# Kernel optimization log

Measured on AMD Instinct MI355X. Metric: run time of the kernel, lower is better.

## Reference

```python
import jax, jax.numpy as jnp
import numpy as np

EPS = 1e-5

def _bn_train(h, gamma, beta):
    # BatchNorm1d in training mode: batch mean and biased variance over batch dim
    mu = jnp.mean(h, axis=0)
    var = jnp.mean((h - mu) ** 2, axis=0)
    return (h - mu) * jax.lax.rsqrt(var + EPS) * gamma + beta

def setup_inputs() -> dict:
    key = jax.random.key(0)
    ks = jax.random.split(key, 12)
    B, IN, H1, H2, NC = 16384, 4096, 256, 128, 12
    x = jax.random.normal(ks[0], (B, 1, 64, 64), dtype=jnp.float32)
    y = jax.random.randint(ks[1], (B,), 0, NC, dtype=jnp.int32)
    s1 = 1.0 / np.sqrt(IN)
    W1 = jax.random.uniform(ks[2], (H1, IN), jnp.float32, -s1, s1)
    b1 = jax.random.uniform(ks[3], (H1,), jnp.float32, -s1, s1)
    g1 = jax.random.normal(ks[4], (H1,), jnp.float32) * 0.1 + 1.0
    be1 = jax.random.normal(ks[5], (H1,), jnp.float32) * 0.1
    s2 = 1.0 / np.sqrt(H1)
    W2 = jax.random.uniform(ks[6], (H2, H1), jnp.float32, -s2, s2)
    b2 = jax.random.uniform(ks[7], (H2,), jnp.float32, -s2, s2)
    g2 = jax.random.normal(ks[8], (H2,), jnp.float32) * 0.1 + 1.0
    be2 = jax.random.normal(ks[9], (H2,), jnp.float32) * 0.1
    s4 = 1.0 / np.sqrt(H2)
    W4 = jax.random.uniform(ks[10], (NC, H2), jnp.float32, -s4, s4)
    b4 = jax.random.uniform(ks[11], (NC,), jnp.float32, -s4, s4)
    return {"x": x, "W1": W1, "b1": b1, "g1": g1, "be1": be1,
            "W2": W2, "b2": b2, "g2": g2, "be2": be2,
            "W4": W4, "b4": b4, "y": y}

def reference(x, W1, b1, g1, be1, W2, b2, g2, be2, W4, b4, y):
    B = x.shape[0]
    h = x.reshape(B, -1)  # [B, 4096]
    # layer 1: binarized linear + BN(train) + hardtanh (dropout p=0 is identity)
    h = h @ jnp.sign(W1).T + jnp.sign(b1)
    h = jnp.clip(_bn_train(h, g1, be1), -1.0, 1.0)
    # layer 2
    h = h @ jnp.sign(W2).T + jnp.sign(b2)
    h = jnp.clip(_bn_train(h, g2, be2), -1.0, 1.0)
    # final float linear
    return h @ W4.T + b4  # [B, 12]
```

## Files before the change

### kernel.cpp

```cpp
#include <hip/hip_runtime.h>
#include <cstddef>

typedef __attribute__((ext_vector_type(8))) short short8;
typedef __attribute__((ext_vector_type(4))) float f4;
typedef __attribute__((ext_vector_type(4))) unsigned int u4;

__device__ __forceinline__ unsigned int f2bf(float f){
  unsigned int u = __float_as_uint(f);
  u += 0x7fffu + ((u >> 16) & 1u);
  return u >> 16;
}
__device__ __forceinline__ float bflo(unsigned int w){ return __uint_as_float((w & 0xFFFFu) << 16); }
__device__ __forceinline__ float bfhi(unsigned int w){ return __uint_as_float(w & 0xFFFF0000u); }
__device__ __forceinline__ float fsign(float x){ return (x > 0.f) ? 1.f : ((x < 0.f) ? -1.f : 0.f); }
__device__ __forceinline__ float hclip(float x){ return fminf(1.f, fmaxf(-1.f, x)); }

#define SB0 __builtin_amdgcn_sched_barrier(0)

#define BARRIER() do { \
    SB0; \
    asm volatile("s_waitcnt lgkmcnt(0)" ::: "memory"); \
    __builtin_amdgcn_s_barrier(); \
    asm volatile("" ::: "memory"); \
    SB0; \
  } while(0)

#define VBAR(N) do { \
    SB0; \
    asm volatile("s_waitcnt vmcnt(" #N ") lgkmcnt(0)" ::: "memory"); \
    __builtin_amdgcn_s_barrier(); \
    asm volatile("" ::: "memory"); \
    SB0; \
  } while(0)

#define GL16(gp, lp) __builtin_amdgcn_global_load_lds( \
    (const __attribute__((address_space(1))) void*)(gp), \
    (__attribute__((address_space(3))) void*)(lp), 16, 0, 0)

__global__ void prep_sign_k(const float* __restrict__ W1, unsigned short* __restrict__ w1s,
                            const float* __restrict__ W2, unsigned short* __restrict__ w2s){
  int i = (blockIdx.x * blockDim.x + threadIdx.x) * 8;
  const float* w; unsigned short* o; int off;
  if (i < 1048576){ w = W1; o = w1s; off = i; }
  else            { w = W2; o = w2s; off = i - 1048576; if (off >= 32768) return; }
  f4 a = *(const f4*)(w + off);
  f4 b = *(const f4*)(w + off + 4);
  unsigned short s[8];
  #pragma unroll
  for (int j = 0; j < 4; j++) s[j]   = (a[j] > 0.f) ? 0x3F80u : ((a[j] < 0.f) ? 0xBF80u : 0u);
  #pragma unroll
  for (int j = 0; j < 4; j++) s[4+j] = (b[j] > 0.f) ? 0x3F80u : ((b[j] < 0.f) ? 0xBF80u : 0u);
  u4 v;
  v.x = (unsigned)s[0] | ((unsigned)s[1] << 16);
  v.y = (unsigned)s[2] | ((unsigned)s[3] << 16);
  v.z = (unsigned)s[4] | ((unsigned)s[5] << 16);
  v.w = (unsigned)s[6] | ((unsigned)s[7] << 16);
  *(u4*)(o + off) = v;
}

__global__ __launch_bounds__(512, 1) void gemm1_k(
    const float* __restrict__ x, const unsigned short* __restrict__ w1s,
    const float* __restrict__ b1, unsigned short* __restrict__ h1,
    float* __restrict__ part1s, float* __restrict__ part1q)
{
  __shared__ __align__(16) char lds[147456];
  const int tid  = threadIdx.x;
  const int lane = tid & 63;
  const int wid  = tid >> 6;
  const int wm   = wid >> 2;
  const int wn   = wid & 3;
  const int cl   = lane & 15;
  const int g    = lane >> 4;
  const int row0 = blockIdx.x * 64;

  const float* xA = x + (size_t)(row0 + (tid >> 3)) * 4096 + (tid & 7) * 8;
  const int aw = (tid >> 3) * 128 + (((tid & 7) * 16) ^ (((tid >> 3) & 7) << 4));

  int afo[2][2], bfo[4][2];
  #pragma unroll
  for (int fm = 0; fm < 2; fm++){
    int m = wm * 32 + fm * 16 + cl;
    #pragma unroll
    for (int ks = 0; ks < 2; ks++)
      afo[fm][ks] = m * 128 + ((ks * 64 + g * 16) ^ ((m & 7) << 4));
  }
  #pragma unroll
  for (int fn = 0; fn < 4; fn++){
    int n = wn * 64 + fn * 16 + cl;
    #pragma unroll
    for (int ks = 0; ks < 2; ks++)
      bfo[fn][ks] = n * 128 + ((ks * 64 + g * 16) ^ ((n & 7) << 4));
  }

  f4 acc[2][4];
  const f4 z = {0.f, 0.f, 0.f, 0.f};
  #pragma unroll
  for (int i = 0; i < 2; i++)
    #pragma unroll
    for (int j = 0; j < 4; j++) acc[i][j] = z;

  f4 rA0a, rA0b, rA1a, rA1b, rA2a, rA2b, rA3a, rA3b;

#define ISSUEA(S, K) do { \
    rA##S##a = *(const f4*)(xA + (size_t)(K) * 64); \
    rA##S##b = *(const f4*)(xA + (size_t)(K) * 64 + 4); \
  } while(0)

#define ISSUEB(BI, K) do { \
    char* _dst = lds + 16384 + (BI) * 32768; \
    _Pragma("unroll") \
    for (int _c = 0; _c < 4; _c++){ \
      int _o  = _c * 8192 + tid * 16; \
      int _n  = _o >> 7; \
      int _kb = (_o & 127) ^ ((_n & 7) << 4); \
      GL16((const char*)w1s + (size_t)_n * 8192 + (size_t)(K) * 128 + _kb, _dst + _o); \
    } } while(0)

#define PACKA(S, AB) do { \
    u4 _v; \
    _v.x = f2bf(rA##S##a[0]) | (f2bf(rA##S##a[1]) << 16); \
    _v.y = f2bf(rA##S##a[2]) | (f2bf(rA##S##a[3]) << 16); \
    _v.z = f2bf(rA##S##b[0]) | (f2bf(rA##S##b[1]) << 16); \
    _v.w = f2bf(rA##S##b[2]) | (f2bf(rA##S##b[3]) << 16); \
    *(u4*)(lds + (AB) * 8192 + aw) = _v; \
  } while(0)

#define COMPUTE(KI) do { \
    const char* _ab = lds + ((KI) & 1) * 8192; \
    const char* _bb = lds + 16384 + ((KI) & 3) * 32768; \
    short8 _af[2][2]; short8 _bf[4][2]; \
    _Pragma("unroll") \
    for (int _fm = 0; _fm < 2; _fm++) \
      _Pragma("unroll") \
      for (int _ks = 0; _ks < 2; _ks++) \
        _af[_fm][_ks] = *(const short8*)(_ab + afo[_fm][_ks]); \
    _Pragma("unroll") \
    for (int _fn = 0; _fn < 4; _fn++) \
      _Pragma("unroll") \
      for (int _ks = 0; _ks < 2; _ks++) \
        _bf[_fn][_ks] = *(const short8*)(_bb + bfo[_fn][_ks]); \
    __builtin_amdgcn_s_setprio(1); \
    _Pragma("unroll") \
    for (int _ks = 0; _ks < 2; _ks++) \
      _Pragma("unroll") \
      for (int _fm = 0; _fm < 2; _fm++) \
        _Pragma("unroll") \
        for (int _fn = 0; _fn < 4; _fn++) \
          acc[_fm][_fn] = __builtin_amdgcn_mfma_f32_16x16x32_bf16(_af[_fm][_ks], _bf[_fn][_ks], acc[_fm][_fn], 0, 0, 0); \
    __builtin_amdgcn_s_setprio(0); \
  } while(0)

#define STEP(K, AS, AP) do { \
    int _kb3 = (K) + 3; if (_kb3 > 63) _kb3 = 63; \
    int _ka4 = (K) + 4; if (_ka4 > 63) _ka4 = 63; \
    ISSUEB((K + 3) & 3, _kb3); \
    ISSUEA(AS, _ka4); \
    SB0; \
    COMPUTE(K); \
    SB0; \
    if ((K) < 63) PACKA(AP, ((K) + 1) & 1); \
    VBAR(14); \
  } while(0)

  ISSUEA(0, 0);
  ISSUEB(0, 0); ISSUEB(1, 1); ISSUEB(2, 2);
  ISSUEA(1, 1); ISSUEA(2, 2); ISSUEA(3, 3);
  SB0;
  PACKA(0, 0);
  VBAR(14);

  #pragma unroll 1
  for (int kk = 0; kk < 64; kk += 4){
    STEP(kk + 0, 0, 1);
    STEP(kk + 1, 1, 2);
    STEP(kk + 2, 2, 3);
    STEP(kk + 3, 3, 0);
  }
  asm volatile("s_waitcnt vmcnt(0)" ::: "memory");

#undef STEP
#undef COMPUTE
#undef PACKA
#undef ISSUEB
#undef ISSUEA

  #pragma unroll
  for (int fn = 0; fn < 4; fn++){
    int c = wn * 64 + fn * 16 + cl;
    float sb = fsign(b1[c]);
    float s = 0.f, q = 0.f;
    #pragma unroll
    for (int fm = 0; fm < 2; fm++){
      int rbase = row0 + wm * 32 + fm * 16 + g * 4;
      #pragma unroll
      for (int i = 0; i < 4; i++){
        float v = acc[fm][fn][i] + sb;
        h1[(size_t)(rbase + i) * 256 + c] = (unsigned short)f2bf(v);
        s += v; q += v * v;
      }
    }
    s += __shfl_xor(s, 16, 64); s += __shfl_xor(s, 32, 64);
    q += __shfl_xor(q, 16, 64); q += __shfl_xor(q, 32, 64);
    if (g == 0){
      part1s[(size_t)c * 512 + blockIdx.x * 2 + wm] = s;
      part1q[(size_t)c * 512 + blockIdx.x * 2 + wm] = q;
    }
  }
}

template<int COLS, int NBLK>
__global__ __launch_bounds__(64) void params_k(
    const float* __restrict__ ps, const float* __restrict__ pq,
    const float* __restrict__ g, const float* __restrict__ be,
    float* __restrict__ ab){
  int j = blockIdx.x * 64 + threadIdx.x;
  const f4* vs = (const f4*)(ps + (size_t)j * NBLK);
  const f4* vq = (const f4*)(pq + (size_t)j * NBLK);
  f4 s4 = {0,0,0,0}, q4 = {0,0,0,0};
  #pragma unroll 8
  for (int b = 0; b < NBLK/4; b++){ s4 += vs[b]; q4 += vq[b]; }
  float s = s4[0]+s4[1]+s4[2]+s4[3];
  float q = q4[0]+q4[1]+q4[2]+q4[3];
  float mu  = s * (1.f/16384.f);
  float var = q * (1.f/16384.f) - mu*mu;
  float a   = g[j] * rsqrtf(var + 1e-5f);
  ab[j] = a;
  ab[COLS + j] = be[j] - mu*a;
}

__global__ __launch_bounds__(512) void gemm2_k(
    const unsigned short* __restrict__ h1, const unsigned short* __restrict__ w2s,
    const float* __restrict__ b2, const float* __restrict__ ab1,
    unsigned short* __restrict__ h2, float* __restrict__ part2s, float* __restrict__ part2q)
{
  __shared__ __align__(16) char lds[32768];
  __shared__ __align__(16) float a1l[256];
  __shared__ __align__(16) float c1l[256];
  const int tid  = threadIdx.x;
  const int lane = tid & 63;
  const int wid  = tid >> 6;
  const int cl   = lane & 15;
  const int g    = lane >> 4;
  const int klo  = g * 8;
  const int row0 = blockIdx.x * 64;

  if (tid < 256) a1l[tid] = ab1[tid];
  else           c1l[tid - 256] = ab1[tid];

  const int am  = tid >> 3;
  const int ak0 = (tid & 7) * 8;
  const unsigned short* hA = h1 + (size_t)(row0 + am) * 256 + ak0;
  const int aw = ((am * 128) + (ak0 * 2)) ^ ((am & 7) << 4);
  const unsigned short* wbase = w2s + (size_t)(wid * 16 + cl) * 256 + klo;

  u4 q0 = *(const u4*)(hA);
  u4 q1 = *(const u4*)(hA + 64);
  u4 q2 = *(const u4*)(hA + 128);
  u4 q3 = *(const u4*)(hA + 192);
  short8 Bq0, Bq1, Br0, Br1;
  Bq0 = *(const short8*)(wbase);
  Bq1 = *(const short8*)(wbase + 32);

  BARRIER();

#define TRW(KB, RAW) do { \
    f4 _a0 = *(const f4*)(&a1l[(KB)*64 + ak0]); \
    f4 _a1 = *(const f4*)(&a1l[(KB)*64 + ak0 + 4]); \
    f4 _c0 = *(const f4*)(&c1l[(KB)*64 + ak0]); \
    f4 _c1 = *(const f4*)(&c1l[(KB)*64 + ak0 + 4]); \
    float _t0 = hclip(_a0[0]*bflo(RAW.x) + _c0[0]); \
    float _t1 = hclip(_a0[1]*bfhi(RAW.x) + _c0[1]); \
    float _t2 = hclip(_a0[2]*bflo(RAW.y) + _c0[2]); \
    float _t3 = hclip(_a0[3]*bfhi(RAW.y) + _c0[3]); \
    float _t4 = hclip(_a1[0]*bflo(RAW.z) + _c1[0]); \
    float _t5 = hclip(_a1[1]*bfhi(RAW.z) + _c1[1]); \
    float _t6 = hclip(_a1[2]*bflo(RAW.w) + _c1[2]); \
    float _t7 = hclip(_a1[3]*bfhi(RAW.w) + _c1[3]); \
    u4 _v; \
    _v.x = f2bf(_t0) | (f2bf(_t1) << 16); \
    _v.y = f2bf(_t2) | (f2bf(_t3) << 16); \
    _v.z = f2bf(_t4) | (f2bf(_t5) << 16); \
    _v.w = f2bf(_t6) | (f2bf(_t7) << 16); \
    *(u4*)(lds + (KB)*8192 + aw) = _v; \
  } while(0)

  TRW(0, q0); TRW(1, q1); TRW(2, q2); TRW(3, q3);
#undef TRW
  BARRIER();

  f4 acc[4];
  const f4 z = {0.f, 0.f, 0.f, 0.f};
  #pragma unroll
  for (int i = 0; i < 4; i++) acc[i] = z;

#define LOADB2(P, KB) do { \
    B##P##0 = *(const short8*)(wbase + (KB)*64); \
    B##P##1 = *(const short8*)(wbase + (KB)*64 + 32); \
  } while(0)

#define COMP2(BASE, P) do { \
    const char* _ab = (const char*)(BASE); \
    short8 _af[4][2]; \
    _Pragma("unroll") \
    for (int fm = 0; fm < 4; fm++){ \
      int _m = fm*16 + cl; \
      _af[fm][0] = *(const short8*)(_ab + ((_m*128 + klo*2) ^ ((_m & 7) << 4))); \
      _af[fm][1] = *(const short8*)(_ab + ((_m*128 + (32 + klo)*2) ^ ((_m & 7) << 4))); \
    } \
    _Pragma("unroll") \
    for (int fm = 0; fm < 4; fm++){ \
      acc[fm] = __builtin_amdgcn_mfma_f32_16x16x32_bf16(_af[fm][0], B##P##0, acc[fm], 0, 0, 0); \
      acc[fm] = __builtin_amdgcn_mfma_f32_16x16x32_bf16(_af[fm][1], B##P##1, acc[fm], 0, 0, 0); \
    } \
  } while(0)

  LOADB2(r, 1);
  COMP2(lds,         q);
  LOADB2(q, 2);
  COMP2(lds +  8192, r);
  LOADB2(r, 3);
  COMP2(lds + 16384, q);
  COMP2(lds + 24576, r);
#undef COMP2
#undef LOADB2

  {
    int c = wid*16 + cl;
    float sb = fsign(b2[c]);
    float s = 0.f, q = 0.f;
    #pragma unroll
    for (int fm = 0; fm < 4; fm++){
      int rbase = row0 + fm*16 + g*4;
      #pragma unroll
      for (int i = 0; i < 4; i++){
        float v = acc[fm][i] + sb;
        h2[(size_t)(rbase + i)*128 + c] = (unsigned short)f2bf(v);
        s += v; q += v*v;
      }
    }
    s += __shfl_xor(s, 16, 64); s += __shfl_xor(s, 32, 64);
    q += __shfl_xor(q, 16, 64); q += __shfl_xor(q, 32, 64);
    if (g == 0){
      part2s[c*256 + blockIdx.x] = s;
      part2q[c*256 + blockIdx.x] = q;
    }
  }
}

__global__ __launch_bounds__(128) void final_k(
    const unsigned short* __restrict__ h2,
    const float* __restrict__ part2s, const float* __restrict__ part2q,
    const float* __restrict__ g2, const float* __restrict__ be2,
    const float* __restrict__ W4, const float* __restrict__ b4,
    float* __restrict__ out)
{
  __shared__ __align__(16) float W4l[12*128];
  __shared__ __align__(16) float a2l[128];
  __shared__ __align__(16) float c2l[128];
  const int t = threadIdx.x;
  #pragma unroll
  for (int i = 0; i < 3; i++)
    *(f4*)&W4l[(i*128 + t)*4] = *(const f4*)(W4 + (i*128 + t)*4);
  {
    const f4* vs = (const f4*)(part2s + t*256);
    const f4* vq = (const f4*)(part2q + t*256);
    f4 s4 = {0,0,0,0}, q4 = {0,0,0,0};
    #pragma unroll 8
    for (int b = 0; b < 64; b++){ s4 += vs[b]; q4 += vq[b]; }
    float s = s4[0]+s4[1]+s4[2]+s4[3];
    float q = q4[0]+q4[1]+q4[2]+q4[3];
    float mu  = s * (1.f/16384.f);
    float var = q * (1.f/16384.f) - mu*mu;
    float a   = g2[t] * rsqrtf(var + 1e-5f);
    a2l[t] = a;
    c2l[t] = be2[t] - mu*a;
  }
  __syncthreads();

  const int r = blockIdx.x * 128 + t;
  const u4* hp = (const u4*)(h2 + (size_t)r * 128);
  u4 hv0 = hp[0], hv1 = hp[1], hv2 = hp[2],  hv3 = hp[3];
  u4 hv4 = hp[4], hv5 = hp[5], hv6 = hp[6],  hv7 = hp[7];
  u4 hv8 = hp[8], hv9 = hp[9], hv10 = hp[10], hv11 = hp[11];
  u4 hv12 = hp[12], hv13 = hp[13], hv14 = hp[14], hv15 = hp[15];

  float acc[12];
  #pragma unroll
  for (int o = 0; o < 12; o++) acc[o] = b4[o];

#define FPROC(HV, J) do { \
    f4 a0 = *(const f4*)&a2l[(J)*8];     f4 a1 = *(const f4*)&a2l[(J)*8 + 4]; \
    f4 c0 = *(const f4*)&c2l[(J)*8];     f4 c1 = *(const f4*)&c2l[(J)*8 + 4]; \
    float tt0 = hclip(a0[0]*bflo(HV.x) + c0[0]); \
    float tt1 = hclip(a0[1]*bfhi(HV.x) + c0[1]); \
    float tt2 = hclip(a0[2]*bflo(HV.y) + c0[2]); \
    float tt3 = hclip(a0[3]*bfhi(HV.y) + c0[3]); \
    float tt4 = hclip(a1[0]*bflo(HV.z) + c1[0]); \
    float tt5 = hclip(a1[1]*bfhi(HV.z) + c1[1]); \
    float tt6 = hclip(a1[2]*bflo(HV.w) + c1[2]); \
    float tt7 = hclip(a1[3]*bfhi(HV.w) + c1[3]); \
    _Pragma("unroll") \
    for (int o = 0; o < 12; o++){ \
      f4 w0 = *(const f4*)&W4l[o*128 + (J)*8]; \
      f4 w1 = *(const f4*)&W4l[o*128 + (J)*8 + 4]; \
      acc[o] += tt0*w0[0] + tt1*w0[1] + tt2*w0[2] + tt3*w0[3] \
              + tt4*w1[0] + tt5*w1[1] + tt6*w1[2] + tt7*w1[3]; \
    } \
  } while(0)

  FPROC(hv0, 0);  FPROC(hv1, 1);  FPROC(hv2, 2);   FPROC(hv3, 3);
  FPROC(hv4, 4);  FPROC(hv5, 5);  FPROC(hv6, 6);   FPROC(hv7, 7);
  FPROC(hv8, 8);  FPROC(hv9, 9);  FPROC(hv10, 10); FPROC(hv11, 11);
  FPROC(hv12, 12); FPROC(hv13, 13); FPROC(hv14, 14); FPROC(hv15, 15);
#undef FPROC

  #pragma unroll
  for (int o = 0; o < 12; o++) out[(size_t)r*12 + o] = acc[o];
}

extern "C" void kernel_launch(void* const* d_in, const int* in_sizes, int n_in,
                              void* d_out, int out_size, void* d_ws, size_t ws_size,
                              hipStream_t stream)
{
  const float* x   = (const float*)d_in[0];
  const float* W1  = (const float*)d_in[1];
  const float* b1  = (const float*)d_in[2];
  const float* g1  = (const float*)d_in[3];
  const float* be1 = (const float*)d_in[4];
  const float* W2  = (const float*)d_in[5];
  const float* b2  = (const float*)d_in[6];
  const float* g2  = (const float*)d_in[7];
  const float* be2 = (const float*)d_in[8];
  const float* W4  = (const float*)d_in[9];
  const float* b4  = (const float*)d_in[10];
  float* out = (float*)d_out;

  char* ws = (char*)d_ws;
  unsigned short* h1     = (unsigned short*)(ws);
  unsigned short* h2     = (unsigned short*)(ws + 8388608);
  unsigned short* w1s    = (unsigned short*)(ws + 12582912);
  unsigned short* w2s    = (unsigned short*)(ws + 14680064);
  float*          part1s = (float*)(ws + 14745600);
  float*          part1q = (float*)(ws + 15269888);
  float*          part2s = (float*)(ws + 15794176);
  float*          part2q = (float*)(ws + 15925248);
  float*          ab1    = (float*)(ws + 16056320);

  prep_sign_k<<<528, 256, 0, stream>>>(W1, w1s, W2, w2s);
  gemm1_k<<<256, 512, 0, stream>>>(x, w1s, b1, h1, part1s, part1q);
  params_k<256, 512><<<4, 64, 0, stream>>>(part1s, part1q, g1, be1, ab1);
  gemm2_k<<<256, 512, 0, stream>>>(h1, w2s, b2, ab1, h2, part2s, part2q);
  final_k<<<128, 128, 0, stream>>>(h2, part2s, part2q, g2, be2, W4, b4, out);
}
```

Before: 117.9 us.

## Split gemm1 output columns across two blocks with shallower pipeline and higher occupancy

Each gemm1 block now computes a 64x128 output tile instead of 64x256, and the grid doubles to 512 blocks. An XCD-aware mapping places both column halves of a row block on the same XCD so they can share L2 hits on x. LDS shrinks from 144KB to 48KB by moving to a 2-stage pipeline with prefetch distance 1–2 for B and A, and launch bounds allow up to 4 blocks per CU. The goal is more parallelism and better latency hiding through occupancy. The cost is that each x row tile is read twice, once per column half, and the shallower software pipeline has less lookahead.

```diff
diff --git a/kernel.cpp b/kernel.cpp
--- a/kernel.cpp
+++ b/kernel.cpp
@@ -58,12 +58,12 @@
   *(u4*)(o + off) = v;
 }
 
-__global__ __launch_bounds__(512, 1) void gemm1_k(
+__global__ __launch_bounds__(512, 4) void gemm1_k(
     const float* __restrict__ x, const unsigned short* __restrict__ w1s,
     const float* __restrict__ b1, unsigned short* __restrict__ h1,
     float* __restrict__ part1s, float* __restrict__ part1q)
 {
-  __shared__ __align__(16) char lds[147456];
+  __shared__ __align__(16) char lds[49152];
   const int tid  = threadIdx.x;
   const int lane = tid & 63;
   const int wid  = tid >> 6;
@@ -71,12 +71,24 @@
   const int wn   = wid & 3;
   const int cl   = lane & 15;
   const int g    = lane >> 4;
-  const int row0 = blockIdx.x * 64;
+  const int d    = blockIdx.x;
+  const int xcd  = d & 7;
+  const int slot = d >> 3;
+  const int nh   = slot & 1;
+  const int gm   = (slot >> 1) * 8 + xcd;
+  const int row0 = gm * 64;
+  const int col0 = nh * 128;
 
   const float* xA = x + (size_t)(row0 + (tid >> 3)) * 4096 + (tid & 7) * 8;
   const int aw = (tid >> 3) * 128 + (((tid & 7) * 16) ^ (((tid >> 3) & 7) << 4));
 
-  int afo[2][2], bfo[4][2];
+  const int o0 = tid * 16;
+  const int o1 = 8192 + tid * 16;
+  const int n0l = o0 >> 7, n1l = o1 >> 7;
+  const size_t sB0 = (size_t)(col0 + n0l) * 8192 + ((o0 & 127) ^ ((n0l & 7) << 4));
+  const size_t sB1 = (size_t)(col0 + n1l) * 8192 + ((o1 & 127) ^ ((n1l & 7) << 4));
+
+  int afo[2][2], bfo[2][2];
   #pragma unroll
   for (int fm = 0; fm < 2; fm++){
     int m = wm * 32 + fm * 16 + cl;
@@ -85,21 +97,18 @@
       afo[fm][ks] = m * 128 + ((ks * 64 + g * 16) ^ ((m & 7) << 4));
   }
   #pragma unroll
-  for (int fn = 0; fn < 4; fn++){
-    int n = wn * 64 + fn * 16 + cl;
+  for (int fn = 0; fn < 2; fn++){
+    int n = wn * 32 + fn * 16 + cl;
     #pragma unroll
     for (int ks = 0; ks < 2; ks++)
       bfo[fn][ks] = n * 128 + ((ks * 64 + g * 16) ^ ((n & 7) << 4));
   }
 
-  f4 acc[2][4];
+  f4 acc[2][2];
   const f4 z = {0.f, 0.f, 0.f, 0.f};
-  #pragma unroll
-  for (int i = 0; i < 2; i++)
-    #pragma unroll
-    for (int j = 0; j < 4; j++) acc[i][j] = z;
-
-  f4 rA0a, rA0b, rA1a, rA1b, rA2a, rA2b, rA3a, rA3b;
+  acc[0][0] = z; acc[0][1] = z; acc[1][0] = z; acc[1][1] = z;
+
+  f4 rA0a, rA0b, rA1a, rA1b;
 
 #define ISSUEA(S, K) do { \
     rA##S##a = *(const f4*)(xA + (size_t)(K) * 64); \
@@ -107,14 +116,10 @@
   } while(0)
 
 #define ISSUEB(BI, K) do { \
-    char* _dst = lds + 16384 + (BI) * 32768; \
-    _Pragma("unroll") \
-    for (int _c = 0; _c < 4; _c++){ \
-      int _o  = _c * 8192 + tid * 16; \
-      int _n  = _o >> 7; \
-      int _kb = (_o & 127) ^ ((_n & 7) << 4); \
-      GL16((const char*)w1s + (size_t)_n * 8192 + (size_t)(K) * 128 + _kb, _dst + _o); \
-    } } while(0)
+    char* _dst = lds + 16384 + (BI) * 16384; \
+    GL16((const char*)w1s + sB0 + (size_t)(K) * 128, _dst + o0); \
+    GL16((const char*)w1s + sB1 + (size_t)(K) * 128, _dst + o1); \
+  } while(0)
 
 #define PACKA(S, AB) do { \
     u4 _v; \
@@ -127,56 +132,60 @@
 
 #define COMPUTE(KI) do { \
     const char* _ab = lds + ((KI) & 1) * 8192; \
-    const char* _bb = lds + 16384 + ((KI) & 3) * 32768; \
-    short8 _af[2][2]; short8 _bf[4][2]; \
-    _Pragma("unroll") \
-    for (int _fm = 0; _fm < 2; _fm++) \
-      _Pragma("unroll") \
-      for (int _ks = 0; _ks < 2; _ks++) \
-        _af[_fm][_ks] = *(const short8*)(_ab + afo[_fm][_ks]); \
-    _Pragma("unroll") \
-    for (int _fn = 0; _fn < 4; _fn++) \
-      _Pragma("unroll") \
-      for (int _ks = 0; _ks < 2; _ks++) \
-        _bf[_fn][_ks] = *(const short8*)(_bb + bfo[_fn][_ks]); \
+    const char* _bb = lds + 16384 + ((KI) & 1) * 16384; \
     __builtin_amdgcn_s_setprio(1); \
-    _Pragma("unroll") \
-    for (int _ks = 0; _ks < 2; _ks++) \
-      _Pragma("unroll") \
-      for (int _fm = 0; _fm < 2; _fm++) \
-        _Pragma("unroll") \
-        for (int _fn = 0; _fn < 4; _fn++) \
-          acc[_fm][_fn] = __builtin_amdgcn_mfma_f32_16x16x32_bf16(_af[_fm][_ks], _bf[_fn][_ks], acc[_fm][_fn], 0, 0, 0); \
+    { \
+      short8 _a0 = *(const short8*)(_ab + afo[0][0]); \
+      short8 _a1 = *(const short8*)(_ab + afo[1][0]); \
+      short8 _b0 = *(const short8*)(_bb + bfo[0][0]); \
+      short8 _b1 = *(const short8*)(_bb + bfo[1][0]); \
+      acc[0][0] = __builtin_amdgcn_mfma_f32_16x16x32_bf16(_a0, _b0, acc[0][0], 0, 0, 0); \
+      acc[0][1] = __builtin_amdgcn_mfma_f32_16x16x32_bf16(_a0, _b1, acc[0][1], 0, 0, 0); \
+      acc[1][0] = __builtin_amdgcn_mfma_f32_16x16x32_bf16(_a1, _b0, acc[1][0], 0, 0, 0); \
+      acc[1][1] = __builtin_amdgcn_mfma_f32_16x16x32_bf16(_a1, _b1, acc[1][1], 0, 0, 0); \
+    } \
+    { \
+      short8 _a0 = *(const short8*)(_ab + afo[0][1]); \
+      short8 _a1 = *(const short8*)(_ab + afo[1][1]); \
+      short8 _b0 = *(const short8*)(_bb + bfo[0][1]); \
+      short8 _b1 = *(const short8*)(_bb + bfo[1][1]); \
+      acc[0][0] = __builtin_amdgcn_mfma_f32_16x16x32_bf16(_a0, _b0, acc[0][0], 0, 0, 0); \
+      acc[0][1] = __builtin_amdgcn_mfma_f32_16x16x32_bf16(_a0, _b1, acc[0][1], 0, 0, 0); \
+      acc[1][0] = __builtin_amdgcn_mfma_f32_16x16x32_bf16(_a1, _b0, acc[1][0], 0, 0, 0); \
+      acc[1][1] = __builtin_amdgcn_mfma_f32_16x16x32_bf16(_a1, _b1, acc[1][1], 0, 0, 0); \
+    } \
     __builtin_amdgcn_s_setprio(0); \
   } while(0)
 
-#define STEP(K, AS, AP) do { \
-    int _kb3 = (K) + 3; if (_kb3 > 63) _kb3 = 63; \
-    int _ka4 = (K) + 4; if (_ka4 > 63) _ka4 = 63; \
-    ISSUEB((K + 3) & 3, _kb3); \
-    ISSUEA(AS, _ka4); \
+#define STEP(K, SI, SP) do { \
+    ISSUEB((K + 1) & 1, (K) + 1); \
+    ISSUEA(SI, (K) + 2); \
     SB0; \
     COMPUTE(K); \
     SB0; \
-    if ((K) < 63) PACKA(AP, ((K) + 1) & 1); \
-    VBAR(14); \
+    PACKA(SP, ((K) + 1) & 1); \
+    VBAR(1); \
   } while(0)
 
   ISSUEA(0, 0);
-  ISSUEB(0, 0); ISSUEB(1, 1); ISSUEB(2, 2);
-  ISSUEA(1, 1); ISSUEA(2, 2); ISSUEA(3, 3);
+  ISSUEB(0, 0);
+  ISSUEA(1, 1);
   SB0;
   PACKA(0, 0);
-  VBAR(14);
+  VBAR(1);
 
   #pragma unroll 1
-  for (int kk = 0; kk < 64; kk += 4){
-    STEP(kk + 0, 0, 1);
-    STEP(kk + 1, 1, 2);
-    STEP(kk + 2, 2, 3);
-    STEP(kk + 3, 3, 0);
-  }
-  asm volatile("s_waitcnt vmcnt(0)" ::: "memory");
+  for (int k = 0; k < 62; k += 2){
+    STEP(k,     0, 1);
+    STEP(k + 1, 1, 0);
+  }
+  ISSUEB(1, 63);
+  SB0;
+  COMPUTE(62);
+  SB0;
+  PACKA(1, 1);
+  VBAR(0);
+  COMPUTE(63);
 
 #undef STEP
 #undef COMPUTE
@@ -185,8 +194,8 @@
 #undef ISSUEA
 
   #pragma unroll
-  for (int fn = 0; fn < 4; fn++){
-    int c = wn * 64 + fn * 16 + cl;
+  for (int fn = 0; fn < 2; fn++){
+    int c = col0 + wn * 32 + fn * 16 + cl;
     float sb = fsign(b1[c]);
     float s = 0.f, q = 0.f;
     #pragma unroll
@@ -202,8 +211,8 @@
     s += __shfl_xor(s, 16, 64); s += __shfl_xor(s, 32, 64);
     q += __shfl_xor(q, 16, 64); q += __shfl_xor(q, 32, 64);
     if (g == 0){
-      part1s[(size_t)c * 512 + blockIdx.x * 2 + wm] = s;
-      part1q[(size_t)c * 512 + blockIdx.x * 2 + wm] = q;
+      part1s[(size_t)c * 512 + gm * 2 + wm] = s;
+      part1q[(size_t)c * 512 + gm * 2 + wm] = q;
     }
   }
 }
@@ -447,7 +456,7 @@
   float*          ab1    = (float*)(ws + 16056320);
 
   prep_sign_k<<<528, 256, 0, stream>>>(W1, w1s, W2, w2s);
-  gemm1_k<<<256, 512, 0, stream>>>(x, w1s, b1, h1, part1s, part1q);
+  gemm1_k<<<512, 512, 0, stream>>>(x, w1s, b1, h1, part1s, part1q);
   params_k<256, 512><<<4, 64, 0, stream>>>(part1s, part1q, g1, be1, ab1);
   gemm2_k<<<256, 512, 0, stream>>>(h1, w2s, b2, ab1, h2, part2s, part2q);
   final_k<<<128, 128, 0, stream>>>(h2, part2s, part2q, g2, be2, W4, b4, out);
```

Measured after the change: 125.7 us. +6.6%, slower.
